# Performance work log

Measured on AMD Instinct MI355X. Metric: run time of the kernel, lower is better.

The kernel has to match this reference:

```python
import jax, jax.numpy as jnp
import numpy as np

B, H_, W_ = 8, 64, 64
N = H_ * W_
IN_DIM = 256
DIM = 256
HEADS = 8
DIM_HEAD = DIM // HEADS      # 32
DH2 = DIM_HEAD // 2          # 16
KC = 3                       # kernel_conv
WS = 8                       # window size
EPS = 1e-5


def _conv2d(x, w, b, groups):
    # x: [B, C, H, W], w: [O, C//groups, kh, kw], 'same' padding, stride 1
    y = jax.lax.conv_general_dilated(
        x, w, window_strides=(1, 1), padding=((1, 1), (1, 1)),
        dimension_numbers=('NCHW', 'OIHW', 'NCHW'), feature_group_count=groups)
    return y + b[None, :, None, None]


def _cross_shaped_attention(q, k, v, H, W, ws, horizontal,
                            fc_w, dep_w, dep_b, rate1, rate2):
    # q, k, v: [B, N, C] with C = dim/2 = 128; H*W == N (no padding path)
    Bq, Nq, C = q.shape
    nh = C // DIM_HEAD  # heads per half = 4
    # ---- parallel conv-attention branch ----
    # [B, 3*heads, dim_head//2, N]
    f = jnp.concatenate([t.reshape(Bq, HEADS, DH2, Nq) for t in (q, k, v)], axis=1)
    # 1x1 conv fc: (heads*3=24) -> (kc*kc=9) channels
    f_all = jnp.einsum('oc,bcst->bost', fc_w, f)           # [B, 9, 16, N]
    f_conv = jnp.transpose(f_all, (0, 2, 1, 3)).reshape(Bq, DH2 * KC * KC, H, W)  # [B,144,H,W]
    out_conv = _conv2d(f_conv, dep_w, dep_b, groups=DH2)   # [B, 128, H, W]
    out_conv = jnp.transpose(out_conv, (0, 2, 3, 1)).reshape(Bq, Nq, C)
    # ---- cross-shaped windowed attention ----
    scale = DIM_HEAD ** -0.5
    if horizontal:
        # window over rows: groups of ws full-width rows -> tokens ws*W
        def win(t):
            t = t.reshape(Bq, H // ws, ws, W, nh, DIM_HEAD)
            return jnp.transpose(t, (0, 1, 4, 2, 3, 5)).reshape(Bq, H // ws, nh, ws * W, DIM_HEAD)
    else:
        # window over cols: groups of ws full-height cols -> tokens ws*H
        def win(t):
            t = t.reshape(Bq, H, W // ws, ws, nh, DIM_HEAD)
            return jnp.transpose(t, (0, 2, 4, 3, 1, 5)).reshape(Bq, W // ws, nh, ws * H, DIM_HEAD)
    qw, kw, vw = win(q), win(k), win(v)
    attn = jnp.einsum('bgnqd,bgnkd->bgnqk', qw, kw) * scale  # [B, G, nh, L, L]
    attn = jax.nn.softmax(attn, axis=-1)
    o = jnp.einsum('bgnqk,bgnkd->bgnqd', attn, vw)           # [B, G, nh, L, dh]
    if horizontal:
        o = o.reshape(Bq, H // ws, nh, ws, W, DIM_HEAD)
        o = jnp.transpose(o, (0, 1, 3, 4, 2, 5)).reshape(Bq, Nq, C)  # B (Hg ws) W (nh dh)
    else:
        o = o.reshape(Bq, W // ws, nh, ws, H, DIM_HEAD)
        o = jnp.transpose(o, (0, 4, 1, 3, 2, 5)).reshape(Bq, Nq, C)  # B H (Wg ws) (nh dh)
    return rate1 * o + rate2 * out_conv


def reference(x, w_qkv, b_qkv, w_out, b_out, bn_g, bn_b, pconv_w, pconv_b,
              fc_w, dep_w, dep_b, rate1, rate2, H, W):
    Bx = x.shape[0]
    Nx = H * W
    qv = x @ w_qkv + b_qkv                       # [B, N, 2*dim]
    q, v = jnp.split(qv, 2, axis=-1)
    # parallel depthwise conv branch on v (hardswish -> dw 3x3)
    v_img = jnp.transpose(v.reshape(Bx, H, W, DIM), (0, 3, 1, 2))
    v_conv = _conv2d(jax.nn.hard_swish(v_img), pconv_w, pconv_b, groups=DIM)
    v_conv = jnp.transpose(v_conv.reshape(Bx, DIM, Nx), (0, 2, 1))   # [B, N, dim]
    qh, qv2 = jnp.split(q, 2, axis=-1)
    vh, vv = jnp.split(v, 2, axis=-1)
    # H % ws == 0 and W % ws == 0 -> no padding, no masks
    attn_h = _cross_shaped_attention(qh, vh, vh, H, W, WS, True,
                                     fc_w, dep_w, dep_b, rate1, rate2)
    attn_v = _cross_shaped_attention(qv2, vv, vv, H, W, WS, False,
                                     fc_w, dep_w, dep_b, rate1, rate2)
    a = jnp.concatenate([attn_h, attn_v], axis=-1) + v_conv
    a = jax.nn.hard_swish(a)
    a = a @ w_out + b_out
    # BatchNorm1d in training mode over flattened (B*N, dim), biased variance
    flat = a.reshape(Bx * Nx, DIM)
    mu = flat.mean(axis=0)
    var = flat.var(axis=0)
    flat = (flat - mu) * jax.lax.rsqrt(var + EPS) * bn_g + bn_b
    return flat.reshape(Bx, Nx, DIM)


def setup_inputs() -> dict:
    key = jax.random.key(0)
    ks = jax.random.split(key, 16)
    s = 0.02
    return {
        'x': jax.random.normal(ks[0], (B, N, IN_DIM), jnp.float32),
        'w_qkv': jax.random.normal(ks[1], (IN_DIM, 2 * DIM), jnp.float32) * s,
        'b_qkv': jax.random.normal(ks[2], (2 * DIM,), jnp.float32) * s,
        'w_out': jax.random.normal(ks[3], (DIM, DIM), jnp.float32) * s,
        'b_out': jax.random.normal(ks[4], (DIM,), jnp.float32) * s,
        'bn_g': jax.random.uniform(ks[5], (DIM,), jnp.float32, 0.5, 1.5),
        'bn_b': jax.random.normal(ks[6], (DIM,), jnp.float32) * s,
        'pconv_w': jax.random.normal(ks[7], (DIM, 1, 3, 3), jnp.float32) * s,
        'pconv_b': jax.random.normal(ks[8], (DIM,), jnp.float32) * s,
        'fc_w': jax.random.normal(ks[9], (KC * KC, HEADS * 3), jnp.float32) * s,
        'dep_w': jax.random.normal(ks[10], (IN_DIM // 2, KC * KC, 3, 3), jnp.float32) * s,
        'dep_b': jax.random.normal(ks[11], (IN_DIM // 2,), jnp.float32) * s,
        'rate1': jax.random.uniform(ks[12], (), jnp.float32, 0.4, 0.6),
        'rate2': jax.random.uniform(ks[13], (), jnp.float32, 0.4, 0.6),
        'H': H_,
        'W': W_,
    }
```

## Files before the change

### kernel.cpp

```cpp
#include <hip/hip_runtime.h>
#include <hip/hip_bf16.h>
#include <math.h>

constexpr int Bn   = 8;
constexpr int Hh   = 64;
constexpr int Ww   = 64;
constexpr int Nn   = Hh * Ww;
constexpr int Mrows = Bn * Nn;
constexpr int QKVC = 512;
constexpr int DIMc = 256;

typedef short short8 __attribute__((ext_vector_type(8)));
typedef float f32x16 __attribute__((ext_vector_type(16)));
typedef float f32x4 __attribute__((ext_vector_type(4)));

__device__ __forceinline__ float hswish(float x) {
    float r = fminf(fmaxf(x + 3.f, 0.f), 6.f);
    return x * r * (1.f / 6.f);
}

__device__ __forceinline__ ushort bf16u(float f) {
    return __bfloat16_as_ushort(__float2bfloat16(f));
}

__device__ __forceinline__ uint32_t pkbf(float a, float b) {
    return (uint32_t)bf16u(a) | ((uint32_t)bf16u(b) << 16);
}

__device__ __forceinline__ float dot2bf(uint32_t a, uint32_t b, float c) {
    asm("v_dot2_f32_bf16 %0, %1, %2, %0" : "+v"(c) : "v"(a), "v"(b));
    return c;
}

__device__ __forceinline__ float bflo(uint32_t p) {
    union { uint32_t u; float f; } c; c.u = p << 16; return c.f;
}
__device__ __forceinline__ float bfhi(uint32_t p) {
    union { uint32_t u; float f; } c; c.u = p & 0xFFFF0000u; return c.f;
}

#if __has_builtin(__builtin_amdgcn_permlane32_swap)
typedef int int2v __attribute__((ext_vector_type(2)));
__device__ __forceinline__ void plswap(uint32_t& a, uint32_t& b) {
    int2v r = __builtin_amdgcn_permlane32_swap((int)a, (int)b, false, false);
    a = (uint32_t)r.x; b = (uint32_t)r.y;
}
#else
__device__ __forceinline__ void plswap(uint32_t& a, uint32_t& b) {
    int l = threadIdx.x & 63;
    uint32_t sa = (uint32_t)__shfl_xor((int)a, 32);
    uint32_t sb = (uint32_t)__shfl_xor((int)b, 32);
    uint32_t na = (l < 32) ? a : sb;
    uint32_t nb = (l < 32) ? sa : b;
    a = na; b = nb;
}
#endif

__device__ __forceinline__ void gload_lds16(const ushort* g, ushort* l) {
    __builtin_amdgcn_global_load_lds(
        (const __attribute__((address_space(1))) unsigned int*)g,
        (__attribute__((address_space(3))) unsigned int*)l, 16, 0, 0);
}

__global__ __launch_bounds__(256) void cvtbf_kernel(
    const float* __restrict__ in, ushort* __restrict__ out)
{
    int i = (blockIdx.x * 256 + threadIdx.x) * 8;
    float4 f0 = *reinterpret_cast<const float4*>(&in[i]);
    float4 f1 = *reinterpret_cast<const float4*>(&in[i + 4]);
    float v[8] = {f0.x, f0.y, f0.z, f0.w, f1.x, f1.y, f1.z, f1.w};
    ushort o[8];
    #pragma unroll
    for (int j = 0; j < 8; ++j) o[j] = bf16u(v[j]);
    *reinterpret_cast<short8*>(&out[i]) = *reinterpret_cast<short8*>(o);
}

__global__ __launch_bounds__(256) void wtconv_kernel(
    const float* __restrict__ Wf, ushort* __restrict__ Wt, int K, int N)
{
    int idx = blockIdx.x * 256 + threadIdx.x;
    int n = idx / K, k = idx - n * K;
    Wt[idx] = bf16u(Wf[(size_t)k * N + n]);
}

__global__ __launch_bounds__(256) void weff_kernel(
    const float* __restrict__ dw, const float* __restrict__ fcw,
    uint32_t* __restrict__ Wp)
{
    int idx = blockIdx.x * 256 + threadIdx.x;
    if (idx >= 9216) return;
    int k = idx % 9;
    int a = (idx / 9) & 7;
    int oc = (idx / 72) & 7;
    int gi = idx / 576;
    float q = 0.f, v = 0.f;
    const float* dwp = &dw[(gi * 8 + oc) * 81 + k];
    #pragma unroll
    for (int ic = 0; ic < 9; ++ic) {
        float d = dwp[ic * 9];
        q += d * fcw[ic * 24 + a];
        v += d * (fcw[ic * 24 + 8 + a] + fcw[ic * 24 + 16 + a]);
    }
    Wp[idx] = pkbf(q, v);
}

template<bool OBF, bool STATS>
__global__ __launch_bounds__(256) void hgemm_kernel(
    const ushort* __restrict__ A, const ushort* __restrict__ Bt,
    const float* __restrict__ bias, void* __restrict__ Cv,
    float* __restrict__ stats, int M, int N, int K)
{
    __shared__ ushort As[128 * 32];
    __shared__ ushort Bs[128 * 32];
    const int tid = threadIdx.x;
    const int w = tid >> 6, l = tid & 63;
    const int brow = blockIdx.y * 128;
    const int bcol = blockIdx.x * 128;
    const int wm = (w >> 1) * 64, wn = (w & 1) * 64;

    f32x4 acc[4][4] = {};

    const int c0 = tid, c1 = tid + 256;
    const int r0 = c0 >> 2, q0 = (c0 & 3) ^ (r0 & 3);
    const int r1 = c1 >> 2, q1 = (c1 & 3) ^ (r1 & 3);
    const ushort* a0p = &A[(size_t)(brow + r0) * K + q0 * 8];
    const ushort* a1p = &A[(size_t)(brow + r1) * K + q1 * 8];
    const ushort* b0p = &Bt[(size_t)(bcol + r0) * K + q0 * 8];
    const ushort* b1p = &Bt[(size_t)(bcol + r1) * K + q1 * 8];
    ushort* asw0 = &As[(w * 64) * 8];
    ushort* asw1 = &As[(256 + w * 64) * 8];
    ushort* bsw0 = &Bs[(w * 64) * 8];
    ushort* bsw1 = &Bs[(256 + w * 64) * 8];

    const int fr = l & 15;
    const int qq = ((l >> 4) ^ (l & 3)) * 8;

    for (int k0 = 0; k0 < K; k0 += 32) {
        gload_lds16(a0p + k0, asw0);
        gload_lds16(a1p + k0, asw1);
        gload_lds16(b0p + k0, bsw0);
        gload_lds16(b1p + k0, bsw1);
        __syncthreads();
        short8 af[4], bf[4];
        #pragma unroll
        for (int i = 0; i < 4; ++i) {
            af[i] = *reinterpret_cast<const short8*>(&As[(wm + i * 16 + fr) * 32 + qq]);
            bf[i] = *reinterpret_cast<const short8*>(&Bs[(wn + i * 16 + fr) * 32 + qq]);
        }
        #pragma unroll
        for (int mi = 0; mi < 4; ++mi)
            #pragma unroll
            for (int ni = 0; ni < 4; ++ni)
                acc[mi][ni] = __builtin_amdgcn_mfma_f32_16x16x32_bf16(
                    af[mi], bf[ni], acc[mi][ni], 0, 0, 0);
        __syncthreads();
    }

    const int cr = l >> 4;
    #pragma unroll
    for (int ni = 0; ni < 4; ++ni) {
        int n = bcol + wn + ni * 16 + fr;
        float bv = bias[n];
        float s1 = 0.f, s2 = 0.f;
        #pragma unroll
        for (int mi = 0; mi < 4; ++mi) {
            int m = brow + wm + mi * 16 + cr * 4;
            #pragma unroll
            for (int r = 0; r < 4; ++r) {
                float val = acc[mi][ni][r] + bv;
                if (OBF)
                    ((ushort*)Cv)[(size_t)(m + r) * N + n] = bf16u(val);
                else
                    ((float*)Cv)[(size_t)(m + r) * N + n] = val;
                if (STATS) { s1 += val; s2 += val * val; }
            }
        }
        if (STATS) {
            s1 += __shfl_xor(s1, 16); s2 += __shfl_xor(s2, 16);
            s1 += __shfl_xor(s1, 32); s2 += __shfl_xor(s2, 32);
            if (cr == 0) {
                atomicAdd(&stats[n], s1);
                atomicAdd(&stats[256 + n], s2);
            }
        }
    }
}

__global__ __launch_bounds__(256) void vconv_kernel(
    const ushort* __restrict__ qvb, const float* __restrict__ pw,
    const float* __restrict__ pb, ushort* __restrict__ Abuf)
{
    int idx = blockIdx.x * 256 + threadIdx.x;
    int c2 = idx & 127;
    int n = (idx >> 7) & (Nn - 1);
    int b = idx >> 19;
    int x = n & 63, y = n >> 6;
    int ch = c2 * 2;
    float s0 = pb[ch], s1 = pb[ch + 1];
    float w0[9], w1[9];
    #pragma unroll
    for (int k = 0; k < 9; ++k) { w0[k] = pw[ch * 9 + k]; w1[k] = pw[ch * 9 + 9 + k]; }
    #pragma unroll
    for (int ky = 0; ky < 3; ++ky) {
        int yy = y + ky - 1;
        if (yy >= 0 && yy < Hh) {
            #pragma unroll
            for (int kx = 0; kx < 3; ++kx) {
                int xx = x + kx - 1;
                if (xx >= 0 && xx < Ww) {
                    uint32_t pk = *reinterpret_cast<const uint32_t*>(
                        &qvb[(size_t)(b * Nn + yy * Ww + xx) * QKVC + 256 + ch]);
                    s0 += hswish(bflo(pk)) * w0[ky * 3 + kx];
                    s1 += hswish(bfhi(pk)) * w1[ky * 3 + kx];
                }
            }
        }
    }
    uint32_t* ap = reinterpret_cast<uint32_t*>(&Abuf[(size_t)(b * Nn + n) * DIMc + ch]);
    uint32_t cur = *ap;
    *ap = pkbf(bflo(cur) + s0, bfhi(cur) + s1);
}

__global__ __launch_bounds__(256) void convbranch_kernel(
    const ushort* __restrict__ qvb, const uint32_t* __restrict__ Wp,
    const float* __restrict__ db, const float* __restrict__ rate2p,
    ushort* __restrict__ Abuf)
{
    int blk = blockIdx.x;
    int ytile = blk & 7;
    int gi = (blk >> 3) & 15;
    int b = (blk >> 7) & 7;
    int branch = blk >> 10;
    int y0 = ytile * 8;
    int qoff = branch * 128;
    int coff = branch * 128;

    __shared__ uint32_t sqv[8][10][68];
    __shared__ uint32_t wpk[8][8][9];
    const int tid = threadIdx.x;

    if (tid < 160) {
        int r = tid >> 1;
        int col = 1 + (tid & 1) * 65;
        sqv[r / 10][r % 10][col] = 0;
    }
    {
        const int x2 = (tid & 31) * 2;
        int rr = tid >> 5;
        int a = 0;
        const size_t bbase = (size_t)(b * Nn) * QKVC + qoff;
        #pragma unroll
        for (int it = 0; it < 10; ++it) {
            int y = y0 + rr - 1;
            uint32_t lo = 0, hi = 0;
            if ((unsigned)y < 64u) {
                int token = (a * 16 + gi) * 32 + (y >> 1);
                size_t base = bbase + (size_t)token * QKVC + (y & 1) * 64 + x2;
                uint32_t q = *reinterpret_cast<const uint32_t*>(&qvb[base]);
                uint32_t v = *reinterpret_cast<const uint32_t*>(&qvb[base + 256]);
                lo = (q & 0xffffu) | (v << 16);
                hi = (q >> 16) | (v & 0xffff0000u);
            }
            uint2 wv; wv.x = lo; wv.y = hi;
            *reinterpret_cast<uint2*>(&sqv[a][rr][2 + x2]) = wv;
            rr += 8;
            if (rr >= 10) { rr -= 10; a += 1; }
        }
    }
    for (int i = tid; i < 576; i += 256)
        ((uint32_t*)wpk)[i] = Wp[gi * 576 + i];
    __syncthreads();

    const int x = tid & 63;
    const int w = tid >> 6;
    const int rh = (w & 1) * 4;
    const int oc0 = (w >> 1) * 4;

    float acc[4][4] = {};
    #pragma unroll 1
    for (int a = 0; a < 8; ++a) {
        uint32_t ipk[6][3];
        #pragma unroll
        for (int j = 0; j < 6; ++j) {
            const uint32_t* rp = &sqv[a][rh + j][1 + x];
            ipk[j][0] = rp[0]; ipk[j][1] = rp[1]; ipk[j][2] = rp[2];
        }
        #pragma unroll
        for (int ocl = 0; ocl < 4; ++ocl) {
            #pragma unroll
            for (int ky = 0; ky < 3; ++ky)
                #pragma unroll
                for (int kx = 0; kx < 3; ++kx) {
                    uint32_t wv = wpk[oc0 + ocl][a][ky * 3 + kx];
                    #pragma unroll
                    for (int ro = 0; ro < 4; ++ro)
                        acc[ocl][ro] = dot2bf(ipk[ro + ky][kx], wv, acc[ocl][ro]);
                }
        }
    }

    const float r2 = rate2p[0];
    float dbv[4];
    #pragma unroll
    for (int j = 0; j < 4; ++j) dbv[j] = db[gi * 8 + oc0 + j];
    #pragma unroll
    for (int ro = 0; ro < 4; ++ro) {
        int n = (y0 + rh + ro) * 64 + x;
        uint2 pk;
        pk.x = pkbf(r2 * (acc[0][ro] + dbv[0]), r2 * (acc[1][ro] + dbv[1]));
        pk.y = pkbf(r2 * (acc[2][ro] + dbv[2]), r2 * (acc[3][ro] + dbv[3]));
        *reinterpret_cast<uint2*>(
            &Abuf[(size_t)(b * Nn + n) * DIMc + coff + gi * 8 + oc0]) = pk;
    }
}

__global__ __launch_bounds__(512) void attn_mfma_kernel(
    const ushort* __restrict__ qvb, const float* __restrict__ rate1p,
    const ushort* __restrict__ Abuf, ushort* __restrict__ Hb)
{
    int bid = blockIdx.x;
    bool hor = bid < 256;
    int lb = bid & 255;
    int hd = lb & 3;
    int g = (lb >> 2) & 7;
    int b = lb >> 5;
    int half = hor ? 0 : 128;
    int qoff = half + hd * 32;
    int kvoff = 256 + qoff;

    __shared__ __align__(16) char smem[65536];
    char* ldsK  = smem;
    char* ldsVT = smem + 32768;

    const int tid = threadIdx.x;
    const float QS = 0.17677669529663687f * 1.44269504088896f;

    {
        int l = tid;
        int n = hor ? (g * 512 + l) : ((l & 63) * 64 + g * 8 + (l >> 6));
        const ushort* kp = &qvb[(size_t)(b * Nn + n) * QKVC + kvoff];
        uint4 wv[4];
        #pragma unroll
        for (int j = 0; j < 4; ++j)
            wv[j] = *reinterpret_cast<const uint4*>(&kp[j * 8]);
        uint32_t p32[16];
        #pragma unroll
        for (int j = 0; j < 4; ++j) {
            p32[j * 4 + 0] = wv[j].x; p32[j * 4 + 1] = wv[j].y;
            p32[j * 4 + 2] = wv[j].z; p32[j * 4 + 3] = wv[j].w;
        }
        #pragma unroll
        for (int gi = 0; gi < 4; ++gi) {
            uint4 w;
            w.x = p32[gi * 4 + 0]; w.y = p32[gi * 4 + 1];
            w.z = p32[gi * 4 + 2]; w.w = p32[gi * 4 + 3];
            *reinterpret_cast<uint4*>(ldsK + l * 64 + ((gi ^ (l & 3)) << 4)) = w;
        }
        #pragma unroll
        for (int d = 0; d < 32; ++d) {
            ushort us = (ushort)((p32[d >> 1] >> ((d & 1) * 16)) & 0xffff);
            *reinterpret_cast<ushort*>(ldsVT + d * 1024 + ((l * 2) ^ ((d & 7) << 4))) = us;
        }
    }
    __syncthreads();

    const int w = tid >> 6;
    const int lane = tid & 63;
    const int qcol = lane & 31;
    const int hh = lane >> 5;
    const float r1 = rate1p[0];

    #pragma unroll 1
    for (int qt = 0; qt < 2; ++qt) {
        const int q0 = (w * 2 + qt) * 32;
        const int qrow = q0 + qcol;
        const int nq = hor ? (g * 512 + qrow) : ((qrow & 63) * 64 + g * 8 + (qrow >> 6));

        short8 qb[2];
        #pragma unroll
        for (int t = 0; t < 2; ++t) {
            const ushort* qp = &qvb[(size_t)(b * Nn + nq) * QKVC + qoff + t * 16 + hh * 8];
            qb[t] = *reinterpret_cast<const short8*>(qp);
        }

        f32x16 acc = {0,0,0,0,0,0,0,0,0,0,0,0,0,0,0,0};
        float rs = 0.f;

        for (int s = 0; s < 16; ++s) {
            const int k0 = s * 32;
            const int kr = k0 + qcol;
            const short8 a0 = *reinterpret_cast<const short8*>(
                ldsK + kr * 64 + (((0 + hh) ^ (kr & 3)) << 4));
            const short8 a1 = *reinterpret_cast<const short8*>(
                ldsK + kr * 64 + (((2 + hh) ^ (kr & 3)) << 4));
            f32x16 st = {0,0,0,0,0,0,0,0,0,0,0,0,0,0,0,0};
            st = __builtin_amdgcn_mfma_f32_32x32x16_bf16(a0, qb[0], st, 0, 0, 0);
            st = __builtin_amdgcn_mfma_f32_32x32x16_bf16(a1, qb[1], st, 0, 0, 0);

            float p[16];
            #pragma unroll
            for (int r = 0; r < 16; ++r) p[r] = exp2f(st[r] * QS);
            float s01 = (p[0] + p[1]) + (p[2] + p[3]);
            float s23 = (p[4] + p[5]) + (p[6] + p[7]);
            float s45 = (p[8] + p[9]) + (p[10] + p[11]);
            float s67 = (p[12] + p[13]) + (p[14] + p[15]);
            rs += (s01 + s23) + (s45 + s67);

            uint32_t X[8];
            #pragma unroll
            for (int gg = 0; gg < 4; ++gg) {
                X[2 * gg + 0] = pkbf(p[4 * gg + 0], p[4 * gg + 1]);
                X[2 * gg + 1] = pkbf(p[4 * gg + 2], p[4 * gg + 3]);
            }
            #pragma unroll
            for (int u = 0; u < 2; ++u) {
                uint32_t w0 = X[4 * u + 0], w2 = X[4 * u + 2];
                uint32_t w1 = X[4 * u + 1], w3 = X[4 * u + 3];
                plswap(w0, w2);
                plswap(w1, w3);
                union { uint32_t u4[4]; short8 s; } pf;
                pf.u4[0] = w0; pf.u4[1] = w1; pf.u4[2] = w2; pf.u4[3] = w3;
                const int d = qcol;
                const short8 vf = *reinterpret_cast<const short8*>(
                    ldsVT + d * 1024 + ((k0 * 2 + u * 32 + hh * 16) ^ ((d & 7) << 4)));
                acc = __builtin_amdgcn_mfma_f32_32x32x16_bf16(vf, pf.s, acc, 0, 0, 0);
            }
        }

        float rsf = rs + __shfl_xor(rs, 32);
        float scl = r1 / rsf;
        const ushort* ap = &Abuf[(size_t)(b * Nn + nq) * DIMc + qoff];
        ushort* hp = &Hb[(size_t)(b * Nn + nq) * DIMc + qoff];
        #pragma unroll
        for (int gg = 0; gg < 4; ++gg) {
            int d0 = 8 * gg + 4 * hh;
            uint2 av = *reinterpret_cast<const uint2*>(&ap[d0]);
            float v0 = hswish(bflo(av.x) + acc[4 * gg + 0] * scl);
            float v1 = hswish(bfhi(av.x) + acc[4 * gg + 1] * scl);
            float v2 = hswish(bflo(av.y) + acc[4 * gg + 2] * scl);
            float v3 = hswish(bfhi(av.y) + acc[4 * gg + 3] * scl);
            uint2 pk; pk.x = pkbf(v0, v1); pk.y = pkbf(v2, v3);
            *reinterpret_cast<uint2*>(&hp[d0]) = pk;
        }
    }
}

__global__ __launch_bounds__(256) void bnnorm_kernel(
    const float* __restrict__ Y, const float* __restrict__ stats,
    const float* __restrict__ g, const float* __restrict__ bta,
    float* __restrict__ out)
{
    int i4 = (blockIdx.x * 256 + threadIdx.x) * 4;
    int c = i4 & 255;
    float4 y = *reinterpret_cast<const float4*>(&Y[i4]);
    float4 mu = *reinterpret_cast<const float4*>(&stats[c]);
    float4 s2 = *reinterpret_cast<const float4*>(&stats[256 + c]);
    float4 gg = *reinterpret_cast<const float4*>(&g[c]);
    float4 bb = *reinterpret_cast<const float4*>(&bta[c]);
    const float inv_m = 1.f / (float)Mrows;
    float4 o;
    {
        float m = mu.x * inv_m, v = s2.x * inv_m - m * m;
        o.x = (y.x - m) * rsqrtf(v + 1e-5f) * gg.x + bb.x;
        m = mu.y * inv_m; v = s2.y * inv_m - m * m;
        o.y = (y.y - m) * rsqrtf(v + 1e-5f) * gg.y + bb.y;
        m = mu.z * inv_m; v = s2.z * inv_m - m * m;
        o.z = (y.z - m) * rsqrtf(v + 1e-5f) * gg.z + bb.z;
        m = mu.w * inv_m; v = s2.w * inv_m - m * m;
        o.w = (y.w - m) * rsqrtf(v + 1e-5f) * gg.w + bb.w;
    }
    *reinterpret_cast<float4*>(&out[i4]) = o;
}

extern "C" void kernel_launch(void* const* d_in, const int* in_sizes, int n_in,
                              void* d_out, int out_size, void* d_ws, size_t ws_size,
                              hipStream_t stream)
{
    const float* x      = (const float*)d_in[0];
    const float* w_qkv  = (const float*)d_in[1];
    const float* b_qkv  = (const float*)d_in[2];
    const float* w_out  = (const float*)d_in[3];
    const float* b_out  = (const float*)d_in[4];
    const float* bn_g   = (const float*)d_in[5];
    const float* bn_b   = (const float*)d_in[6];
    const float* pconv_w = (const float*)d_in[7];
    const float* pconv_b = (const float*)d_in[8];
    const float* fc_w   = (const float*)d_in[9];
    const float* dep_w  = (const float*)d_in[10];
    const float* dep_b  = (const float*)d_in[11];
    const float* rate1  = (const float*)d_in[12];
    const float* rate2  = (const float*)d_in[13];
    float* out = (float*)d_out;

    char* ws = (char*)d_ws;
    ushort* qvb   = (ushort*)(ws);
    ushort* Hb    = (ushort*)(ws + (32u << 20));
    ushort* Abuf  = (ushort*)(ws + (48u << 20));
    ushort* xb    = (ushort*)(ws + (64u << 20));
    float*  Ybuf  = (float*)(ws + (96u << 20));
    float*  stats = (float*)(ws + (128u << 20));
    ushort* Wt1   = (ushort*)(ws + (128u << 20) + 4096);
    ushort* Wt2   = (ushort*)(ws + (128u << 20) + 4096 + (256u << 10));
    uint32_t* Wp  = (uint32_t*)(ws + (128u << 20) + 4096 + (384u << 10));

    wtconv_kernel<<<(512 * 256) / 256, 256, 0, stream>>>(w_qkv, Wt1, 256, 512);
    wtconv_kernel<<<(256 * 256) / 256, 256, 0, stream>>>(w_out, Wt2, 256, 256);
    weff_kernel<<<36, 256, 0, stream>>>(dep_w, fc_w, Wp);
    cvtbf_kernel<<<(Mrows * 256 / 8) / 256, 256, 0, stream>>>(x, xb);

    hgemm_kernel<true, false><<<dim3(4, 256), 256, 0, stream>>>(
        xb, Wt1, b_qkv, qvb, nullptr, Mrows, 512, 256);

    convbranch_kernel<<<2048, 256, 0, stream>>>(qvb, Wp, dep_b, rate2, Abuf);

    vconv_kernel<<<(Mrows * 128) / 256, 256, 0, stream>>>(qvb, pconv_w, pconv_b, Abuf);

    attn_mfma_kernel<<<512, 512, 0, stream>>>(qvb, rate1, Abuf, Hb);

    hipMemsetAsync(stats, 0, 2 * 256 * sizeof(float), stream);
    hgemm_kernel<false, true><<<dim3(2, 256), 256, 0, stream>>>(
        Hb, Wt2, b_out, Ybuf, stats, Mrows, 256, 256);

    bnnorm_kernel<<<(Mrows * 256 / 4) / 256, 256, 0, stream>>>(Ybuf, stats, bn_g, bn_b, out);
}
```

Measured before the change: 200.9 us.

## Rework attention LDS staging layout, prescale Q, and use hardware bf16 pack

The K tile is stored in LDS with a new pair-row swizzle. The V transpose now writes 32-bit words built from lane pairs via shuffle instead of 16-bit scalar stores, which cuts the LDS store count during staging. Q is pre-multiplied by the softmax scale (with log2e folded in) before being fed to MFMA, removing a multiply per score element. Software bf16 packing is replaced with the v_cvt_pk_bf16_f32 instruction, and LDS address math is hoisted out of the inner loop. Rounding Q to bf16 after scaling slightly changes numerics.

```diff
diff --git a/kernel.cpp b/kernel.cpp
--- a/kernel.cpp
+++ b/kernel.cpp
@@ -25,6 +25,12 @@
 
 __device__ __forceinline__ uint32_t pkbf(float a, float b) {
     return (uint32_t)bf16u(a) | ((uint32_t)bf16u(b) << 16);
+}
+
+__device__ __forceinline__ uint32_t cvtpk(float a, float b) {
+    uint32_t r;
+    asm("v_cvt_pk_bf16_f32 %0, %1, %2" : "=v"(r) : "v"(a), "v"(b));
+    return r;
 }
 
 __device__ __forceinline__ float dot2bf(uint32_t a, uint32_t b, float c) {
@@ -339,27 +345,30 @@
         int l = tid;
         int n = hor ? (g * 512 + l) : ((l & 63) * 64 + g * 8 + (l >> 6));
         const ushort* kp = &qvb[(size_t)(b * Nn + n) * QKVC + kvoff];
-        uint4 wv[4];
-        #pragma unroll
-        for (int j = 0; j < 4; ++j)
-            wv[j] = *reinterpret_cast<const uint4*>(&kp[j * 8]);
         uint32_t p32[16];
         #pragma unroll
         for (int j = 0; j < 4; ++j) {
-            p32[j * 4 + 0] = wv[j].x; p32[j * 4 + 1] = wv[j].y;
-            p32[j * 4 + 2] = wv[j].z; p32[j * 4 + 3] = wv[j].w;
-        }
-        #pragma unroll
-        for (int gi = 0; gi < 4; ++gi) {
+            uint4 wv = *reinterpret_cast<const uint4*>(&kp[j * 8]);
+            p32[j * 4 + 0] = wv.x; p32[j * 4 + 1] = wv.y;
+            p32[j * 4 + 2] = wv.z; p32[j * 4 + 3] = wv.w;
+        }
+        const int kpair = l >> 1, hf = l & 1;
+        #pragma unroll
+        for (int gc = 0; gc < 4; ++gc) {
+            int cp = (hf * 4 + gc) ^ (kpair & 7);
             uint4 w;
-            w.x = p32[gi * 4 + 0]; w.y = p32[gi * 4 + 1];
-            w.z = p32[gi * 4 + 2]; w.w = p32[gi * 4 + 3];
-            *reinterpret_cast<uint4*>(ldsK + l * 64 + ((gi ^ (l & 3)) << 4)) = w;
-        }
-        #pragma unroll
-        for (int d = 0; d < 32; ++d) {
-            ushort us = (ushort)((p32[d >> 1] >> ((d & 1) * 16)) & 0xffff);
-            *reinterpret_cast<ushort*>(ldsVT + d * 1024 + ((l * 2) ^ ((d & 7) << 4))) = us;
+            w.x = p32[gc * 4 + 0]; w.y = p32[gc * 4 + 1];
+            w.z = p32[gc * 4 + 2]; w.w = p32[gc * 4 + 3];
+            *reinterpret_cast<uint4*>(ldsK + kpair * 128 + cp * 16) = w;
+        }
+        #pragma unroll
+        for (int j = 0; j < 16; ++j) {
+            uint32_t other = (uint32_t)__shfl_xor((int)p32[j], 1);
+            uint32_t pk = hf ? ((other >> 16) | (p32[j] & 0xffff0000u))
+                             : ((p32[j] & 0xffffu) | (other << 16));
+            int d = 2 * j + hf;
+            *reinterpret_cast<uint32_t*>(
+                ldsVT + d * 1024 + ((kpair * 4) ^ ((d & 7) << 4))) = pk;
         }
     }
     __syncthreads();
@@ -369,6 +378,15 @@
     const int qcol = lane & 31;
     const int hh = lane >> 5;
     const float r1 = rate1p[0];
+    const f32x16 fz = {0,0,0,0,0,0,0,0,0,0,0,0,0,0,0,0};
+
+    const int kp0 = qcol >> 1;
+    const char* pK = ldsK + kp0 * 128;
+    const int ca0 = ((((qcol & 1) * 4) + hh) ^ (kp0 & 7)) * 16;
+    const int ca1 = ((((qcol & 1) * 4) + 2 + hh) ^ (kp0 & 7)) * 16;
+    const int dvt = qcol;
+    const char* pVT = ldsVT + dvt * 1024;
+    const int vtx = (hh * 16) ^ ((dvt & 7) << 4);
 
     #pragma unroll 1
     for (int qt = 0; qt < 2; ++qt) {
@@ -376,30 +394,31 @@
         const int qrow = q0 + qcol;
         const int nq = hor ? (g * 512 + qrow) : ((qrow & 63) * 64 + g * 8 + (qrow >> 6));
 
-        short8 qb[2];
+        short8 qs[2];
         #pragma unroll
         for (int t = 0; t < 2; ++t) {
             const ushort* qp = &qvb[(size_t)(b * Nn + nq) * QKVC + qoff + t * 16 + hh * 8];
-            qb[t] = *reinterpret_cast<const short8*>(qp);
-        }
-
-        f32x16 acc = {0,0,0,0,0,0,0,0,0,0,0,0,0,0,0,0};
+            uint4 raw = *reinterpret_cast<const uint4*>(qp);
+            union { uint32_t u[4]; short8 s; } qa;
+            qa.u[0] = cvtpk(bflo(raw.x) * QS, bfhi(raw.x) * QS);
+            qa.u[1] = cvtpk(bflo(raw.y) * QS, bfhi(raw.y) * QS);
+            qa.u[2] = cvtpk(bflo(raw.z) * QS, bfhi(raw.z) * QS);
+            qa.u[3] = cvtpk(bflo(raw.w) * QS, bfhi(raw.w) * QS);
+            qs[t] = qa.s;
+        }
+
+        f32x16 acc = fz;
         float rs = 0.f;
 
         for (int s = 0; s < 16; ++s) {
-            const int k0 = s * 32;
-            const int kr = k0 + qcol;
-            const short8 a0 = *reinterpret_cast<const short8*>(
-                ldsK + kr * 64 + (((0 + hh) ^ (kr & 3)) << 4));
-            const short8 a1 = *reinterpret_cast<const short8*>(
-                ldsK + kr * 64 + (((2 + hh) ^ (kr & 3)) << 4));
-            f32x16 st = {0,0,0,0,0,0,0,0,0,0,0,0,0,0,0,0};
-            st = __builtin_amdgcn_mfma_f32_32x32x16_bf16(a0, qb[0], st, 0, 0, 0);
-            st = __builtin_amdgcn_mfma_f32_32x32x16_bf16(a1, qb[1], st, 0, 0, 0);
+            const short8 a0 = *reinterpret_cast<const short8*>(pK + s * 2048 + ca0);
+            const short8 a1 = *reinterpret_cast<const short8*>(pK + s * 2048 + ca1);
+            f32x16 st = __builtin_amdgcn_mfma_f32_32x32x16_bf16(a0, qs[0], fz, 0, 0, 0);
+            st = __builtin_amdgcn_mfma_f32_32x32x16_bf16(a1, qs[1], st, 0, 0, 0);
 
             float p[16];
             #pragma unroll
-            for (int r = 0; r < 16; ++r) p[r] = exp2f(st[r] * QS);
+            for (int r = 0; r < 16; ++r) p[r] = exp2f(st[r]);
             float s01 = (p[0] + p[1]) + (p[2] + p[3]);
             float s23 = (p[4] + p[5]) + (p[6] + p[7]);
             float s45 = (p[8] + p[9]) + (p[10] + p[11]);
@@ -409,9 +428,10 @@
             uint32_t X[8];
             #pragma unroll
             for (int gg = 0; gg < 4; ++gg) {
-                X[2 * gg + 0] = pkbf(p[4 * gg + 0], p[4 * gg + 1]);
-                X[2 * gg + 1] = pkbf(p[4 * gg + 2], p[4 * gg + 3]);
+                X[2 * gg + 0] = cvtpk(p[4 * gg + 0], p[4 * gg + 1]);
+                X[2 * gg + 1] = cvtpk(p[4 * gg + 2], p[4 * gg + 3]);
             }
+            const int k0 = s * 32;
             #pragma unroll
             for (int u = 0; u < 2; ++u) {
                 uint32_t w0 = X[4 * u + 0], w2 = X[4 * u + 2];
@@ -420,9 +440,8 @@
                 plswap(w1, w3);
                 union { uint32_t u4[4]; short8 s; } pf;
                 pf.u4[0] = w0; pf.u4[1] = w1; pf.u4[2] = w2; pf.u4[3] = w3;
-                const int d = qcol;
                 const short8 vf = *reinterpret_cast<const short8*>(
-                    ldsVT + d * 1024 + ((k0 * 2 + u * 32 + hh * 16) ^ ((d & 7) << 4)));
+                    pVT + ((k0 * 2 + u * 32) ^ vtx));
                 acc = __builtin_amdgcn_mfma_f32_32x32x16_bf16(vf, pf.s, acc, 0, 0, 0);
             }
         }
@@ -439,7 +458,7 @@
             float v1 = hswish(bfhi(av.x) + acc[4 * gg + 1] * scl);
             float v2 = hswish(bflo(av.y) + acc[4 * gg + 2] * scl);
             float v3 = hswish(bfhi(av.y) + acc[4 * gg + 3] * scl);
-            uint2 pk; pk.x = pkbf(v0, v1); pk.y = pkbf(v2, v3);
+            uint2 pk; pk.x = cvtpk(v0, v1); pk.y = cvtpk(v2, v3);
             *reinterpret_cast<uint2*>(&hp[d0]) = pk;
         }
     }
```

After: 193.3 us. 1.04x faster.
